# Kernel optimization log

Measured on AMD Instinct MI355X. Metric: run time of the kernel, lower is better.

Reference implementation:

```python
import jax, jax.numpy as jnp
import numpy as np

N_NODES = 100000
N_EDGES = 6400000
HID = 64
NEG_SLOPE = 0.2  # GATConv default negative_slope


def _glorot(key, shape, scale=0.1):
    return scale * jax.random.normal(key, shape, dtype=jnp.float32)


def setup_inputs() -> dict:
    key = jax.random.key(0)
    ks = jax.random.split(key, 16)
    x = jax.random.normal(ks[0], (N_NODES, 1), dtype=jnp.float32)
    edge_index = jax.random.randint(ks[1], (2, N_EDGES), 0, N_NODES, dtype=jnp.int64)
    edge_weight = jax.random.uniform(ks[2], (N_EDGES,), dtype=jnp.float32)
    # layer 0: 1 -> 64
    W0 = _glorot(ks[3], (1, HID))
    as0 = _glorot(ks[4], (HID,))
    ad0 = _glorot(ks[5], (HID,))
    b0 = jnp.zeros((HID,), dtype=jnp.float32)
    Wm = _glorot(ks[6], (3, HID, HID))
    asm_ = _glorot(ks[7], (3, HID))
    adm = _glorot(ks[8], (3, HID))
    bm = jnp.zeros((3, HID), dtype=jnp.float32)
    # last layer: 64 -> 1
    WL = _glorot(ks[9], (HID, 1))
    asL = _glorot(ks[10], (1,))
    adL = _glorot(ks[11], (1,))
    bL = jnp.zeros((1,), dtype=jnp.float32)
    return {"x": x, "edge_index": edge_index, "edge_weight": edge_weight,
            "W0": W0, "as0": as0, "ad0": ad0, "b0": b0,
            "Wm": Wm, "asm_": asm_, "adm": adm, "bm": bm,
            "WL": WL, "asL": asL, "adL": adL, "bL": bL}


def _gat_layer(x, src, dst, W, a_s, a_d, b, n_nodes):
    # x: [N, Cin] -> h: [N, Cout]; heads=1, concat=False
    h = x @ W
    e = (h @ a_s)[src] + (h @ a_d)[dst]            # [E] attention logits per edge
    e = jnp.where(e > 0, e, NEG_SLOPE * e)          # LeakyReLU(0.2)
    m = jax.ops.segment_max(e, dst, num_segments=n_nodes)
    ex = jnp.exp(e - m[dst])                        # stable per-dst softmax
    denom = jax.ops.segment_sum(ex, dst, num_segments=n_nodes)
    alpha = ex / denom[dst]                         # [E]
    out = jax.ops.segment_sum(alpha[:, None] * h[src], dst, num_segments=n_nodes)
    return out + b


def reference(x, edge_index, edge_weight, W0, as0, ad0, b0, Wm, asm_, adm, bm, WL, asL, adL, bL):
    # edge_weight is routed to GATConv's edge_attr; with edge_dim=None it is ignored.
    n = x.shape[0]
    loops = jnp.arange(n, dtype=edge_index.dtype)   # GATConv add_self_loops=True
    src = jnp.concatenate([edge_index[0], loops])
    dst = jnp.concatenate([edge_index[1], loops])
    h = jax.nn.relu(_gat_layer(x, src, dst, W0, as0, ad0, b0, n))
    for i in range(Wm.shape[0]):
        h = jax.nn.relu(_gat_layer(h, src, dst, Wm[i], asm_[i], adm[i], bm[i], n))
    out = jax.nn.sigmoid(_gat_layer(h, src, dst, WL, asL, adL, bL, n))
    return out  # [N, 1]
```

## Files before the change

### kernel.cpp

```cpp
#include <hip/hip_runtime.h>
#include <math.h>

#define HID 64
#define NEG 0.2f
#define BSH 9
#define BNODES 512
#define CH 16384
#define NBMAX 256

typedef float f32x2 __attribute__((ext_vector_type(2)));
typedef float f32x4 __attribute__((ext_vector_type(4)));
typedef __bf16 bfx8 __attribute__((ext_vector_type(8)));

__global__ void transform0_k(const float* __restrict__ xin,
                             const float* __restrict__ W,
                             const float* __restrict__ avs,
                             const float* __restrict__ avd,
                             unsigned char* __restrict__ hf8,
                             float* __restrict__ s_out, float* __restrict__ d_out,
                             int n) {
    __shared__ float Wl[HID];
    __shared__ float asl[HID], adl[HID];
    if (threadIdx.x < HID) {
        Wl[threadIdx.x] = W[threadIdx.x];
        asl[threadIdx.x] = avs[threadIdx.x];
        adl[threadIdx.x] = avd[threadIdx.x];
    }
    __syncthreads();
    int lane = threadIdx.x & 63;
    int wid = (blockIdx.x * blockDim.x + threadIdx.x) >> 6;
    int nw = (gridDim.x * blockDim.x) >> 6;
    for (int i = wid; i < n; i += nw) {
        float hv = xin[i] * Wl[lane];
        int pk = __builtin_amdgcn_cvt_pk_fp8_f32(hv, hv, 0, false);
        hf8[(size_t)i * HID + lane] = (unsigned char)(pk & 0xff);
        float sv = hv * asl[lane], dv = hv * adl[lane];
#pragma unroll
        for (int off = 32; off > 0; off >>= 1) {
            sv += __shfl_xor(sv, off);
            dv += __shfl_xor(dv, off);
        }
        if (lane == 0) { s_out[i] = sv; d_out[i] = dv; }
    }
}

__global__ __launch_bounds__(256) void transform_mfma_k(
    const float* __restrict__ xin,
    const float* __restrict__ W,
    const float* __restrict__ avs, const float* __restrict__ avd,
    unsigned char* __restrict__ hf8,
    float* __restrict__ s_out, float* __restrict__ d_out,
    int n) {
    __shared__ bfx8 wfrag[8][64];
    int t = threadIdx.x;
    int lane = t & 63;
    int wsub = t >> 6;
    int m = lane & 15, g = lane >> 4;
#pragma unroll
    for (int cc = 0; cc < 2; ++cc) {
        int co = wsub * 2 + cc;
        int ks = co >> 2, nt = co & 3;
        int c = 4 * m + nt;
        bfx8 f;
#pragma unroll
        for (int j = 0; j < 8; ++j) {
            int k = ks * 32 + g * 8 + j;
            f[j] = (__bf16)W[k * 64 + c];
        }
        wfrag[co][lane] = f;
    }
    __syncthreads();
    float4 as4 = *(const float4*)&avs[4 * m];
    float4 ad4 = *(const float4*)&avd[4 * m];
    int ntiles = (n + 15) >> 4;
    int wid = (blockIdx.x * blockDim.x + t) >> 6;
    int nw = (gridDim.x * blockDim.x) >> 6;
    for (int tile = wid; tile < ntiles; tile += nw) {
        int node0 = tile << 4;
        int row = node0 + m;
        int rl = row < n ? row : n - 1;
        const float* ap = xin + (size_t)rl * HID + g * 8;
        float4 x0 = *(const float4*)ap;
        float4 x1 = *(const float4*)(ap + 4);
        float4 x2 = *(const float4*)(ap + 32);
        float4 x3 = *(const float4*)(ap + 36);
        bfx8 a0, a1;
        a0[0] = (__bf16)x0.x; a0[1] = (__bf16)x0.y; a0[2] = (__bf16)x0.z; a0[3] = (__bf16)x0.w;
        a0[4] = (__bf16)x1.x; a0[5] = (__bf16)x1.y; a0[6] = (__bf16)x1.z; a0[7] = (__bf16)x1.w;
        a1[0] = (__bf16)x2.x; a1[1] = (__bf16)x2.y; a1[2] = (__bf16)x2.z; a1[3] = (__bf16)x2.w;
        a1[4] = (__bf16)x3.x; a1[5] = (__bf16)x3.y; a1[6] = (__bf16)x3.z; a1[7] = (__bf16)x3.w;
        f32x4 ac0 = {0.f, 0.f, 0.f, 0.f}, ac1 = {0.f, 0.f, 0.f, 0.f};
        f32x4 ac2 = {0.f, 0.f, 0.f, 0.f}, ac3 = {0.f, 0.f, 0.f, 0.f};
        ac0 = __builtin_amdgcn_mfma_f32_16x16x32_bf16(a0, wfrag[0][lane], ac0, 0, 0, 0);
        ac1 = __builtin_amdgcn_mfma_f32_16x16x32_bf16(a0, wfrag[1][lane], ac1, 0, 0, 0);
        ac2 = __builtin_amdgcn_mfma_f32_16x16x32_bf16(a0, wfrag[2][lane], ac2, 0, 0, 0);
        ac3 = __builtin_amdgcn_mfma_f32_16x16x32_bf16(a0, wfrag[3][lane], ac3, 0, 0, 0);
        ac0 = __builtin_amdgcn_mfma_f32_16x16x32_bf16(a1, wfrag[4][lane], ac0, 0, 0, 0);
        ac1 = __builtin_amdgcn_mfma_f32_16x16x32_bf16(a1, wfrag[5][lane], ac1, 0, 0, 0);
        ac2 = __builtin_amdgcn_mfma_f32_16x16x32_bf16(a1, wfrag[6][lane], ac2, 0, 0, 0);
        ac3 = __builtin_amdgcn_mfma_f32_16x16x32_bf16(a1, wfrag[7][lane], ac3, 0, 0, 0);
#pragma unroll
        for (int i = 0; i < 4; ++i) {
            int r = node0 + g * 4 + i;
            if (r < n) {
                unsigned w32 = (unsigned)__builtin_amdgcn_cvt_pk_fp8_f32(ac0[i], ac1[i], 0, false);
                w32 = (unsigned)__builtin_amdgcn_cvt_pk_fp8_f32(ac2[i], ac3[i], (int)w32, true);
                *(unsigned*)&hf8[(size_t)r * HID + 4 * m] = w32;
            }
            float ps = ac0[i] * as4.x + ac1[i] * as4.y + ac2[i] * as4.z + ac3[i] * as4.w;
            float pd = ac0[i] * ad4.x + ac1[i] * ad4.y + ac2[i] * ad4.z + ac3[i] * ad4.w;
#pragma unroll
            for (int o = 1; o < 16; o <<= 1) {
                ps += __shfl_xor(ps, o);
                pd += __shfl_xor(pd, o);
            }
            if (m == 0 && r < n) { s_out[r] = ps; d_out[r] = pd; }
        }
    }
}

__global__ void transform_last_k(const float* __restrict__ xin,
                                 const float* __restrict__ WL,
                                 const float* __restrict__ asL, const float* __restrict__ adL,
                                 float2* __restrict__ sh2,
                                 float* __restrict__ d_out,
                                 int n) {
    __shared__ float Wl[HID];
    if (threadIdx.x < HID) Wl[threadIdx.x] = WL[threadIdx.x];
    __syncthreads();
    float aS = asL[0], aD = adL[0];
    int lane = threadIdx.x & 63;
    int wid = (blockIdx.x * blockDim.x + threadIdx.x) >> 6;
    int nw = (gridDim.x * blockDim.x) >> 6;
    for (int i = wid; i < n; i += nw) {
        float hv = xin[(size_t)i * HID + lane] * Wl[lane];
#pragma unroll
        for (int off = 32; off > 0; off >>= 1) hv += __shfl_xor(hv, off);
        if (lane == 0) {
            sh2[i] = make_float2(hv * aS, hv);
            d_out[i] = hv * aD;
        }
    }
}

__global__ __launch_bounds__(256) void chunk_hist_k(const int* __restrict__ ei, int E, int nb,
                                                    int* __restrict__ counts) {
    __shared__ int lh[NBMAX];
    int t = threadIdx.x;
    int base = blockIdx.x * CH;
    int end = base + CH; if (end > E) end = E;
    for (int b = t; b < NBMAX; b += 256) lh[b] = 0;
    __syncthreads();
    for (int e = base + t; e < end; e += 256)
        atomicAdd(&lh[ei[E + e] >> BSH], 1);
    __syncthreads();
    for (int b = t; b < nb; b += 256)
        counts[(size_t)blockIdx.x * nb + b] = lh[b];
}

__global__ void col_scan_k(int* __restrict__ counts, int nchunks, int nb,
                           int* __restrict__ total) {
    int b = (blockIdx.x * blockDim.x + threadIdx.x) >> 6;
    int lane = threadIdx.x & 63;
    if (b >= nb) return;
    int run = 0;
    for (int c0 = 0; c0 < nchunks; c0 += 64) {
        int c = c0 + lane;
        int v = (c < nchunks) ? counts[(size_t)c * nb + b] : 0;
        int inc = v;
#pragma unroll
        for (int o = 1; o < 64; o <<= 1) {
            int w = __shfl_up(inc, o);
            if (lane >= o) inc += w;
        }
        int excl = inc - v + run;
        if (c < nchunks) counts[(size_t)c * nb + b] = excl;
        run += __shfl(inc, 63);
    }
    if (lane == 0) total[b] = run;
}

__global__ void bucket_scan_k(const int* __restrict__ total, int* __restrict__ pbase, int nb) {
    __shared__ int s[1024];
    int t = threadIdx.x;
    int v = (t < nb) ? total[t] : 0;
    s[t] = v;
    __syncthreads();
    for (int o = 1; o < 1024; o <<= 1) {
        int x = (t >= o) ? s[t - o] : 0;
        __syncthreads();
        s[t] += x;
        __syncthreads();
    }
    if (t < nb) {
        pbase[t] = s[t] - v;
        if (t == nb - 1) pbase[nb] = s[t];
    }
}

__global__ __launch_bounds__(256) void chunk_scatter_k(const int* __restrict__ ei, int E, int nb,
                                                       const int* __restrict__ counts,
                                                       const int* __restrict__ pbase,
                                                       unsigned* __restrict__ pairs) {
    __shared__ int lcur[NBMAX];
    int t = threadIdx.x;
    int c = blockIdx.x;
    int base = c * CH;
    int end = base + CH; if (end > E) end = E;
    for (int b = t; b < nb; b += 256)
        lcur[b] = pbase[b] + counts[(size_t)c * nb + b];
    __syncthreads();
    for (int e = base + t; e < end; e += 256) {
        int u = ei[e], v = ei[E + e];
        int b = v >> BSH;
        int pos = atomicAdd(&lcur[b], 1);
        pairs[pos] = ((unsigned)u << BSH) | (unsigned)(v & (BNODES - 1));
    }
}

__global__ __launch_bounds__(512) void csr_build_k(const unsigned* __restrict__ pairs,
                                                   const int* __restrict__ pbase,
                                                   int nb, int n,
                                                   int* __restrict__ off, int* __restrict__ csr) {
    __shared__ int cnt[BNODES];
    __shared__ int sc[BNODES];
    __shared__ int cur[BNODES];
    int b = blockIdx.x;
    int pb = pbase[b], pe = pbase[b + 1];
    int node0 = b << BSH;
    int nnode = n - node0; if (nnode > BNODES) nnode = BNODES;
    int cbase = pb + node0;
    int t = threadIdx.x;
    cnt[t] = 0;
    __syncthreads();
    for (int i = pb + t; i < pe; i += blockDim.x)
        atomicAdd(&cnt[pairs[i] & (BNODES - 1)], 1);
    __syncthreads();
    int deg = (t < nnode) ? cnt[t] + 1 : 0;
    sc[t] = deg;
    __syncthreads();
#pragma unroll
    for (int o = 1; o < BNODES; o <<= 1) {
        int x = (t >= o) ? sc[t - o] : 0;
        __syncthreads();
        sc[t] += x;
        __syncthreads();
    }
    if (t < nnode) {
        int excl = sc[t] - deg;
        off[node0 + t] = cbase + excl;
        cur[t] = excl;
        csr[cbase + excl + cnt[t]] = node0 + t;
    }
    if (b == nb - 1 && t == 0) off[n] = cbase + sc[BNODES - 1];
    __syncthreads();
    for (int i = pb + t; i < pe; i += blockDim.x) {
        unsigned p = pairs[i];
        int j = p & (BNODES - 1);
        int pos = atomicAdd(&cur[j], 1);
        csr[cbase + pos] = (int)(p >> BSH);
    }
}

__global__ __launch_bounds__(256, 8) void gat_agg_k(
    const int* __restrict__ off, const int* __restrict__ csr,
    const float* __restrict__ s, const float* __restrict__ d,
    const unsigned char* __restrict__ hf8, const float* __restrict__ b,
    float* __restrict__ out, int n) {
    __shared__ uint2 eu_lds[4][128];
    int lane = threadIdx.x & 63;
    int wsub = threadIdx.x >> 6;
    int sub = lane & 7;
    int q = lane >> 3;
    int ch = sub * 8;
    int wid = (blockIdx.x * blockDim.x + threadIdx.x) >> 6;
    int nw = (gridDim.x * blockDim.x) >> 6;
    uint2* eup = eu_lds[wsub];
    float4 bb0 = *(const float4*)&b[ch];
    float4 bb1 = *(const float4*)&b[ch + 4];

#define GAT_FMA(EU, HV)                                                     \
    {                                                                       \
        f32x2 E;                                                            \
        E.x = __uint_as_float((EU).x); E.y = E.x;                           \
        a01 += E * (f32x2)__builtin_amdgcn_cvt_pk_f32_fp8((HV).x, false);   \
        a23 += E * (f32x2)__builtin_amdgcn_cvt_pk_f32_fp8((HV).x, true);    \
        a45 += E * (f32x2)__builtin_amdgcn_cvt_pk_f32_fp8((HV).y, false);   \
        a67 += E * (f32x2)__builtin_amdgcn_cvt_pk_f32_fp8((HV).y, true);    \
    }

    for (int v = wid; v < n; v += nw) {
        int beg = off[v];
        int deg = off[v + 1] - beg;
        float dv = d[v];
        float l = 0.f;
        f32x2 a01 = {0.f, 0.f}, a23 = {0.f, 0.f}, a45 = {0.f, 0.f}, a67 = {0.f, 0.f};
        for (int base = 0; base < deg; base += 128) {
            int rem = deg - base;
            int kmax = rem < 128 ? rem : 128;
            unsigned ua = 0u, ub = 0u;
            float ea = 0.f, eb = 0.f;
            bool va = lane < kmax, vb = lane + 64 < kmax;
            if (va) ua = (unsigned)csr[beg + base + lane];
            if (vb) ub = (unsigned)csr[beg + base + 64 + lane];
            float sa = va ? s[ua] : 0.f;
            float sb = vb ? s[ub] : 0.f;
            if (va) {
                float t = sa + dv;
                t = t > 0.f ? t : NEG * t;
                ea = __expf(t);
            }
            if (vb) {
                float t = sb + dv;
                t = t > 0.f ? t : NEG * t;
                eb = __expf(t);
            }
            l += ea + eb;
            eup[lane] = make_uint2(__float_as_uint(ea), ua);
            eup[64 + lane] = make_uint2(__float_as_uint(eb), ub);
            int k0 = 0;
            for (; k0 + 32 <= kmax; k0 += 32) {
                uint2 e0 = eup[k0 + q];
                uint2 e1 = eup[k0 + q + 8];
                uint2 e2 = eup[k0 + q + 16];
                uint2 e3 = eup[k0 + q + 24];
                uint2 h0 = *(const uint2*)&hf8[(size_t)e0.y * HID + ch];
                uint2 h1 = *(const uint2*)&hf8[(size_t)e1.y * HID + ch];
                uint2 h2 = *(const uint2*)&hf8[(size_t)e2.y * HID + ch];
                uint2 h3 = *(const uint2*)&hf8[(size_t)e3.y * HID + ch];
                GAT_FMA(e0, h0) GAT_FMA(e1, h1) GAT_FMA(e2, h2) GAT_FMA(e3, h3)
            }
            for (; k0 < kmax; k0 += 8) {
                uint2 e0 = eup[k0 + q];
                uint2 h0 = *(const uint2*)&hf8[(size_t)e0.y * HID + ch];
                GAT_FMA(e0, h0)
            }
        }
#pragma unroll
        for (int o = 8; o < 64; o <<= 1) {
            a01.x += __shfl_xor(a01.x, o); a01.y += __shfl_xor(a01.y, o);
            a23.x += __shfl_xor(a23.x, o); a23.y += __shfl_xor(a23.y, o);
            a45.x += __shfl_xor(a45.x, o); a45.y += __shfl_xor(a45.y, o);
            a67.x += __shfl_xor(a67.x, o); a67.y += __shfl_xor(a67.y, o);
        }
#pragma unroll
        for (int o = 1; o < 64; o <<= 1) l += __shfl_xor(l, o);
        if (q == 0) {
            float inv = 1.f / l;
            float4 r0, r1;
            r0.x = a01.x * inv + bb0.x; r0.y = a01.y * inv + bb0.y;
            r0.z = a23.x * inv + bb0.z; r0.w = a23.y * inv + bb0.w;
            r1.x = a45.x * inv + bb1.x; r1.y = a45.y * inv + bb1.y;
            r1.z = a67.x * inv + bb1.z; r1.w = a67.y * inv + bb1.w;
            r0.x = r0.x > 0.f ? r0.x : 0.f; r0.y = r0.y > 0.f ? r0.y : 0.f;
            r0.z = r0.z > 0.f ? r0.z : 0.f; r0.w = r0.w > 0.f ? r0.w : 0.f;
            r1.x = r1.x > 0.f ? r1.x : 0.f; r1.y = r1.y > 0.f ? r1.y : 0.f;
            r1.z = r1.z > 0.f ? r1.z : 0.f; r1.w = r1.w > 0.f ? r1.w : 0.f;
            *(float4*)&out[(size_t)v * HID + ch] = r0;
            *(float4*)&out[(size_t)v * HID + ch + 4] = r1;
        }
    }
#undef GAT_FMA
}

__global__ void gat_agg1_k(const int* __restrict__ off, const int* __restrict__ csr,
                           const float2* __restrict__ sh2, const float* __restrict__ d,
                           const float* __restrict__ bL,
                           float* __restrict__ out, int n) {
    int lane = threadIdx.x & 63;
    int wid = (blockIdx.x * blockDim.x + threadIdx.x) >> 6;
    int nw = (gridDim.x * blockDim.x) >> 6;
    float bias = bL[0];
    for (int v = wid; v < n; v += nw) {
        int beg = off[v], end = off[v + 1];
        float dv = d[v];
        float l = 0.f, acc = 0.f;
        int i = beg + lane;
        for (; i + 192 < end; i += 256) {
            int u0 = csr[i], u1 = csr[i + 64], u2 = csr[i + 128], u3 = csr[i + 192];
            float2 p0 = sh2[u0], p1 = sh2[u1], p2 = sh2[u2], p3 = sh2[u3];
            float t0 = p0.x + dv, t1 = p1.x + dv, t2 = p2.x + dv, t3 = p3.x + dv;
            t0 = t0 > 0.f ? t0 : NEG * t0; t1 = t1 > 0.f ? t1 : NEG * t1;
            t2 = t2 > 0.f ? t2 : NEG * t2; t3 = t3 > 0.f ? t3 : NEG * t3;
            float e0 = __expf(t0), e1 = __expf(t1), e2 = __expf(t2), e3 = __expf(t3);
            l += e0 + e1 + e2 + e3;
            acc += e0 * p0.y + e1 * p1.y + e2 * p2.y + e3 * p3.y;
        }
        for (; i < end; i += 64) {
            int u = csr[i];
            float2 p = sh2[u];
            float t = p.x + dv;
            t = t > 0.f ? t : NEG * t;
            float e = __expf(t);
            l += e;
            acc += e * p.y;
        }
#pragma unroll
        for (int o = 32; o > 0; o >>= 1) {
            l += __shfl_xor(l, o);
            acc += __shfl_xor(acc, o);
        }
        if (lane == 0) {
            float r = acc / l + bias;
            out[v] = 1.f / (1.f + __expf(-r));
        }
    }
}

extern "C" void kernel_launch(void* const* d_in, const int* in_sizes, int n_in,
                              void* d_out, int out_size, void* d_ws, size_t ws_size,
                              hipStream_t stream) {
    const float* x   = (const float*)d_in[0];
    const int*   ei  = (const int*)d_in[1];
    const float* W0  = (const float*)d_in[3];
    const float* as0 = (const float*)d_in[4];
    const float* ad0 = (const float*)d_in[5];
    const float* b0  = (const float*)d_in[6];
    const float* Wm  = (const float*)d_in[7];
    const float* asm_ = (const float*)d_in[8];
    const float* adm = (const float*)d_in[9];
    const float* bm  = (const float*)d_in[10];
    const float* WL  = (const float*)d_in[11];
    const float* asL = (const float*)d_in[12];
    const float* adL = (const float*)d_in[13];
    const float* bL  = (const float*)d_in[14];

    const int n = in_sizes[0];
    const int E = in_sizes[1] / 2;
    const int nb = (n + BNODES - 1) >> BSH;
    const int gChunk = (E + CH - 1) / CH;

    float* ws   = (float*)d_ws;
    float* h    = ws;
    unsigned char* hf8 = (unsigned char*)ws;
    float2* sh2 = (float2*)ws;
    float* A    = ws + (size_t)n * HID;
    float* sbuf = ws + 2 * (size_t)n * HID;
    float* dbuf = sbuf + n;
    int* off    = (int*)(dbuf + n);
    int* csr    = off + n + 1;
    int* total  = csr + E + n;
    int* pbase  = total + nb;
    int* counts = (int*)h;
    unsigned* pairs = (unsigned*)A;

    const int BLK = 256;
    const int gTrans = 2048;
    const int gAgg   = (n + 3) / 4;
    const int ntiles = (n + 15) >> 4;
    const int gMfma  = (ntiles + 3) / 4;

    chunk_hist_k<<<gChunk, BLK, 0, stream>>>(ei, E, nb, counts);
    col_scan_k<<<(nb + 3) / 4, BLK, 0, stream>>>(counts, gChunk, nb, total);
    bucket_scan_k<<<1, 1024, 0, stream>>>(total, pbase, nb);
    chunk_scatter_k<<<gChunk, BLK, 0, stream>>>(ei, E, nb, counts, pbase, pairs);
    csr_build_k<<<nb, 512, 0, stream>>>(pairs, pbase, nb, n, off, csr);

    transform0_k<<<gTrans, BLK, 0, stream>>>(x, W0, as0, ad0, hf8, sbuf, dbuf, n);
    gat_agg_k<<<gAgg, BLK, 0, stream>>>(off, csr, sbuf, dbuf, hf8, b0, A, n);

    for (int l = 0; l < 3; ++l) {
        transform_mfma_k<<<gMfma, BLK, 0, stream>>>(A, Wm + (size_t)l * HID * HID,
                                                    asm_ + l * HID, adm + l * HID,
                                                    hf8, sbuf, dbuf, n);
        gat_agg_k<<<gAgg, BLK, 0, stream>>>(off, csr, sbuf, dbuf, hf8, bm + l * HID, A, n);
    }

    transform_last_k<<<gTrans, BLK, 0, stream>>>(A, WL, asL, adL, sh2, dbuf, n);
    gat_agg1_k<<<gAgg, BLK, 0, stream>>>(off, csr, sh2, dbuf, bL, (float*)d_out, n);
}
```

Baseline: 713.0 us.

## Prefetch next node's CSR indices and source scores in the 64-wide aggregation

The wave-per-node aggregation loop is software-pipelined. Offsets, degree, the first 128 neighbour indices and their source scores for the next node are loaded before the current node's gather loop runs, so their latency overlaps with the FMA work. Neighbour indices are also pre-shifted by 6 and stored that way, which turns the row address into a 32-bit add instead of a 64-bit multiply. The cost is more live registers, which may lower occupancy, and 32-bit offsets that assume N*64 fits in an unsigned int.

Result: slower. 817.6 us (+14.7%).

```diff
diff --git a/kernel.cpp b/kernel.cpp
--- a/kernel.cpp
+++ b/kernel.cpp
@@ -288,51 +288,101 @@
         a45 += E * (f32x2)__builtin_amdgcn_cvt_pk_f32_fp8((HV).y, false);   \
         a67 += E * (f32x2)__builtin_amdgcn_cvt_pk_f32_fp8((HV).y, true);    \
     }
-
-    for (int v = wid; v < n; v += nw) {
-        int beg = off[v];
-        int deg = off[v + 1] - beg;
-        float dv = d[v];
-        float l = 0.f;
+#define GAT_LD(EU) (*(const uint2*)(hf8 + ((EU).y + (unsigned)ch)))
+
+    int v = wid;
+    int beg = 0, deg = 0;
+    float dvv = 0.f, sa = 0.f, sb = 0.f;
+    unsigned ua = 0u, ub = 0u;
+    if (v < n) {
+        beg = off[v];
+        deg = off[v + 1] - beg;
+        dvv = d[v];
+        int km = deg < 128 ? deg : 128;
+        if (lane < km) { ua = (unsigned)csr[beg + lane]; sa = s[ua]; }
+        if (lane + 64 < km) { ub = (unsigned)csr[beg + 64 + lane]; sb = s[ub]; }
+    }
+    while (v < n) {
+        int vn = v + nw;
+        int km = deg < 128 ? deg : 128;
+        float ea = 0.f, eb = 0.f;
+        if (lane < km) {
+            float t = sa + dvv;
+            t = t > 0.f ? t : NEG * t;
+            ea = __expf(t);
+        }
+        if (lane + 64 < km) {
+            float t = sb + dvv;
+            t = t > 0.f ? t : NEG * t;
+            eb = __expf(t);
+        }
+        float l = ea + eb;
+        eup[lane] = make_uint2(__float_as_uint(ea), ua << 6);
+        eup[64 + lane] = make_uint2(__float_as_uint(eb), ub << 6);
+        int beg2 = 0, deg2 = 0;
+        float dv2 = 0.f, sa2 = 0.f, sb2 = 0.f;
+        unsigned ua2 = 0u, ub2 = 0u;
+        if (vn < n) {
+            beg2 = off[vn];
+            deg2 = off[vn + 1] - beg2;
+            dv2 = d[vn];
+            int km2 = deg2 < 128 ? deg2 : 128;
+            if (lane < km2) { ua2 = (unsigned)csr[beg2 + lane]; sa2 = s[ua2]; }
+            if (lane + 64 < km2) { ub2 = (unsigned)csr[beg2 + 64 + lane]; sb2 = s[ub2]; }
+        }
         f32x2 a01 = {0.f, 0.f}, a23 = {0.f, 0.f}, a45 = {0.f, 0.f}, a67 = {0.f, 0.f};
-        for (int base = 0; base < deg; base += 128) {
+        int k0 = 0;
+        for (; k0 + 32 <= km; k0 += 32) {
+            uint2 e0 = eup[k0 + q];
+            uint2 e1 = eup[k0 + q + 8];
+            uint2 e2 = eup[k0 + q + 16];
+            uint2 e3 = eup[k0 + q + 24];
+            uint2 h0 = GAT_LD(e0);
+            uint2 h1 = GAT_LD(e1);
+            uint2 h2 = GAT_LD(e2);
+            uint2 h3 = GAT_LD(e3);
+            GAT_FMA(e0, h0) GAT_FMA(e1, h1) GAT_FMA(e2, h2) GAT_FMA(e3, h3)
+        }
+        for (; k0 < km; k0 += 8) {
+            uint2 e0 = eup[k0 + q];
+            uint2 h0 = GAT_LD(e0);
+            GAT_FMA(e0, h0)
+        }
+        for (int base = 128; base < deg; base += 128) {
             int rem = deg - base;
             int kmax = rem < 128 ? rem : 128;
-            unsigned ua = 0u, ub = 0u;
-            float ea = 0.f, eb = 0.f;
-            bool va = lane < kmax, vb = lane + 64 < kmax;
-            if (va) ua = (unsigned)csr[beg + base + lane];
-            if (vb) ub = (unsigned)csr[beg + base + 64 + lane];
-            float sa = va ? s[ua] : 0.f;
-            float sb = vb ? s[ub] : 0.f;
-            if (va) {
-                float t = sa + dv;
+            unsigned fa = 0u, fb = 0u;
+            float fea = 0.f, feb = 0.f;
+            if (lane < kmax) {
+                fa = (unsigned)csr[beg + base + lane];
+                float t = s[fa] + dvv;
                 t = t > 0.f ? t : NEG * t;
-                ea = __expf(t);
+                fea = __expf(t);
             }
-            if (vb) {
-                float t = sb + dv;
+            if (lane + 64 < kmax) {
+                fb = (unsigned)csr[beg + base + 64 + lane];
+                float t = s[fb] + dvv;
                 t = t > 0.f ? t : NEG * t;
-                eb = __expf(t);
+                feb = __expf(t);
             }
-            l += ea + eb;
-            eup[lane] = make_uint2(__float_as_uint(ea), ua);
-            eup[64 + lane] = make_uint2(__float_as_uint(eb), ub);
-            int k0 = 0;
-            for (; k0 + 32 <= kmax; k0 += 32) {
-                uint2 e0 = eup[k0 + q];
-                uint2 e1 = eup[k0 + q + 8];
-                uint2 e2 = eup[k0 + q + 16];
-                uint2 e3 = eup[k0 + q + 24];
-                uint2 h0 = *(const uint2*)&hf8[(size_t)e0.y * HID + ch];
-                uint2 h1 = *(const uint2*)&hf8[(size_t)e1.y * HID + ch];
-                uint2 h2 = *(const uint2*)&hf8[(size_t)e2.y * HID + ch];
-                uint2 h3 = *(const uint2*)&hf8[(size_t)e3.y * HID + ch];
+            l += fea + feb;
+            eup[lane] = make_uint2(__float_as_uint(fea), fa << 6);
+            eup[64 + lane] = make_uint2(__float_as_uint(feb), fb << 6);
+            int kk = 0;
+            for (; kk + 32 <= kmax; kk += 32) {
+                uint2 e0 = eup[kk + q];
+                uint2 e1 = eup[kk + q + 8];
+                uint2 e2 = eup[kk + q + 16];
+                uint2 e3 = eup[kk + q + 24];
+                uint2 h0 = GAT_LD(e0);
+                uint2 h1 = GAT_LD(e1);
+                uint2 h2 = GAT_LD(e2);
+                uint2 h3 = GAT_LD(e3);
                 GAT_FMA(e0, h0) GAT_FMA(e1, h1) GAT_FMA(e2, h2) GAT_FMA(e3, h3)
             }
-            for (; k0 < kmax; k0 += 8) {
-                uint2 e0 = eup[k0 + q];
-                uint2 h0 = *(const uint2*)&hf8[(size_t)e0.y * HID + ch];
+            for (; kk < kmax; kk += 8) {
+                uint2 e0 = eup[kk + q];
+                uint2 h0 = GAT_LD(e0);
                 GAT_FMA(e0, h0)
             }
         }
@@ -359,7 +409,11 @@
             *(float4*)&out[(size_t)v * HID + ch] = r0;
             *(float4*)&out[(size_t)v * HID + ch + 4] = r1;
         }
-    }
+        v = vn;
+        beg = beg2; deg = deg2; dvv = dv2;
+        ua = ua2; ub = ub2; sa = sa2; sb = sb2;
+    }
+#undef GAT_LD
 #undef GAT_FMA
 }
 
```
